# Kernel tuning notes

Measured on AMD Instinct MI355X. Metric: run time of the kernel, lower is better.

The kernel has to match this reference:

```python
import jax, jax.numpy as jnp
import numpy as np

B, TY, ENC, EMB, DEC, V = 16, 255, 512, 256, 512, 32000
EPS = 1e-5


def _lstm(x, Wih, Whh, bih, bhh):
    # x: [B, T, Din]; torch gate order i, f, g, o; h0 = c0 = 0
    Bb = x.shape[0]
    H = Whh.shape[1]
    xw = jnp.einsum('btd,gd->btg', x, Wih) + bih + bhh  # [B, T, 4H]

    def step(carry, xt):
        h, c = carry
        g = xt + h @ Whh.T
        i, f, gg, o = jnp.split(g, 4, axis=-1)
        i = jax.nn.sigmoid(i)
        f = jax.nn.sigmoid(f)
        gg = jnp.tanh(gg)
        o = jax.nn.sigmoid(o)
        c = f * c + i * gg
        h = o * jnp.tanh(c)
        return (h, c), h

    h0 = jnp.zeros((Bb, H), x.dtype)
    _, hs = jax.lax.scan(step, (h0, h0), jnp.swapaxes(xw, 0, 1))
    return jnp.swapaxes(hs, 0, 1)  # [B, T, H]


def setup_inputs():
    key = jax.random.key(0)
    ks = jax.random.split(key, 16)
    s = 0.05
    rn = lambda k, sh: jax.random.normal(k, sh, jnp.float32)
    return {
        'x': rn(ks[0], (B, ENC)),
        'y': jax.random.randint(ks[1], (B, TY), 0, V),
        'fc1_w': rn(ks[2], (EMB, ENC)) * s,
        'fc1_b': rn(ks[3], (EMB,)) * s,
        'bn_g': jnp.ones((EMB,), jnp.float32),
        'bn_b': jnp.zeros((EMB,), jnp.float32),
        'emb': rn(ks[4], (V, EMB)) * s,
        'l1_Wih': rn(ks[5], (4 * DEC, EMB)) * s,
        'l1_Whh': rn(ks[6], (4 * DEC, DEC)) * s,
        'l1_bih': rn(ks[7], (4 * DEC,)) * s,
        'l1_bhh': rn(ks[8], (4 * DEC,)) * s,
        'attn_Wout': rn(ks[9], (DEC, 2 * DEC)) * s,
        'dc_Wih': rn(ks[10], (4 * DEC, DEC)) * s,
        'dc_Whh': rn(ks[11], (4 * DEC, DEC)) * s,
        'dc_bih': rn(ks[12], (4 * DEC,)) * s,
        'dc_bhh': rn(ks[13], (4 * DEC,)) * s,
        'fc2_w': rn(ks[14], (V, DEC)) * s,
        'fc2_b': rn(ks[15], (V,)) * s,
        'lengths': TY + 1,  # all sequences full length
    }


def reference(x, y, fc1_w, fc1_b, bn_g, bn_b, emb, l1_Wih, l1_Whh, l1_bih, l1_bhh,
              attn_Wout, dc_Wih, dc_Whh, dc_bih, dc_bhh, fc2_w, fc2_b, lengths):
    # fc1 + BatchNorm1d (training-mode batch stats, biased var)
    feat = x @ fc1_w.T + fc1_b                         # [B, EMB]
    mu = feat.mean(axis=0)
    var = feat.var(axis=0)
    feat = (feat - mu) / jnp.sqrt(var + EPS) * bn_g + bn_b
    # prepend feature to embedded tokens -> [B, L, EMB], L = TY + 1
    seq = jnp.concatenate([feat[:, None, :], emb[y]], axis=1)
    # first LSTM
    h = _lstm(seq, l1_Wih, l1_Whh, l1_bih, l1_bhh)     # [B, L, DEC]
    L = seq.shape[1]
    # causal dot-product self-attention (vectorized form of the python loop)
    scores = jnp.einsum('bqd,bkd->bqk', h, h)
    mask = jnp.tril(jnp.ones((L, L), bool))
    w = jax.nn.softmax(jnp.where(mask, scores, -1e30), axis=-1)
    mix = jnp.einsum('bqk,bkd->bqd', w, h)
    attn = jnp.tanh(jnp.concatenate([mix, h], axis=-1) @ attn_Wout.T)
    # decoder LSTM cell over attended features
    out = _lstm(attn, dc_Wih, dc_Whh, dc_bih, dc_bhh)  # [B, L, DEC]
    return out @ fc2_w.T + fc2_b                       # [B, L, V]
```

## Files before the change

kernel.cpp:

```cpp
#include <hip/hip_runtime.h>

#define BB 16
#define TY 255
#define ENC 512
#define EMBD 256
#define DEC 512
#define VV 32000
#define LL 256
#define M4 4096
#define GG 2048
#define SENT 0x7FC0

typedef unsigned short u16;
typedef __attribute__((ext_vector_type(8))) short short8;
typedef __attribute__((ext_vector_type(4))) float f32x4;
typedef __attribute__((ext_vector_type(4))) unsigned short u16x4;

__device__ __forceinline__ u16 f2bf(float f) {
  unsigned u = __float_as_uint(f);
  u += 0x7fff + ((u >> 16) & 1);
  return (u16)(u >> 16);
}
__device__ __forceinline__ f32x4 mfma16(short8 a, short8 b, f32x4 c) {
  return __builtin_amdgcn_mfma_f32_16x16x32_bf16(a, b, c, 0, 0, 0);
}
__device__ __forceinline__ float sigmoidf_(float x) { return 1.f / (1.f + expf(-x)); }

__device__ __forceinline__ void st_b32_dev(int* a, int v) {
  asm volatile("global_store_dword %0, %1, off sc1" :: "v"(a), "v"(v) : "memory");
}
__device__ __forceinline__ void gload_lds16(const u16* g, u16* l) {
  __builtin_amdgcn_global_load_lds(
      (const __attribute__((address_space(1))) void*)g,
      (__attribute__((address_space(3))) void*)l, 16, 0, 0);
}

template<bool BT, bool OBF, bool DOTANH, bool BIAS>
__global__ __launch_bounds__(256) void gemm_kernel(
    const u16* __restrict__ A, const u16* __restrict__ Bm, void* __restrict__ Cv,
    const float* __restrict__ bias,
    int K, int lda, int ldb, int ldc,
    long a_bs, long b_bs, long c_bs)
{
  __shared__ u16 As[64][72];
  __shared__ u16 Bs[64][72];
  const int tid = threadIdx.x;
  const long m0 = (long)blockIdx.y * 64, n0 = (long)blockIdx.x * 64;
  const int z = blockIdx.z;
  const u16* Ab = A + (long)z * a_bs;
  const u16* Bb = Bm + (long)z * b_bs;
  const int lane = tid & 63, w = tid >> 6;
  const int wm = w >> 1, wn = w & 1;
  f32x4 acc[2][2] = {};
  for (int k0 = 0; k0 < K; k0 += 64) {
#pragma unroll
    for (int i = 0; i < 2; i++) {
      int c = tid + 256 * i;
      int r = c >> 3, kk = (c & 7) << 3;
      *(short8*)&As[r][kk] = *(const short8*)&Ab[(m0 + r) * (long)lda + k0 + kk];
    }
    if (BT) {
#pragma unroll
      for (int i = 0; i < 2; i++) {
        int c = tid + 256 * i;
        int r = c >> 3, kk = (c & 7) << 3;
        *(short8*)&Bs[r][kk] = *(const short8*)&Bb[(n0 + r) * (long)ldb + k0 + kk];
      }
    } else {
#pragma unroll
      for (int i = 0; i < 2; i++) {
        int c = tid + 256 * i;
        int kk = c >> 3, nn = (c & 7) << 3;
        const u16* s = &Bb[(long)(k0 + kk) * ldb + n0 + nn];
#pragma unroll
        for (int j = 0; j < 8; j++) Bs[nn + j][kk] = s[j];
      }
    }
    __syncthreads();
#pragma unroll
    for (int kf = 0; kf < 2; kf++) {
      const int ko = kf * 32 + (lane >> 4) * 8;
      short8 a0 = *(const short8*)&As[wm * 32 + (lane & 15)][ko];
      short8 a1 = *(const short8*)&As[wm * 32 + 16 + (lane & 15)][ko];
      short8 b0 = *(const short8*)&Bs[wn * 32 + (lane & 15)][ko];
      short8 b1 = *(const short8*)&Bs[wn * 32 + 16 + (lane & 15)][ko];
      acc[0][0] = mfma16(a0, b0, acc[0][0]);
      acc[0][1] = mfma16(a0, b1, acc[0][1]);
      acc[1][0] = mfma16(a1, b0, acc[1][0]);
      acc[1][1] = mfma16(a1, b1, acc[1][1]);
    }
    __syncthreads();
  }
#pragma unroll
  for (int m = 0; m < 2; m++)
#pragma unroll
    for (int n = 0; n < 2; n++) {
#pragma unroll
      for (int r = 0; r < 4; r++) {
        long row = m0 + wm * 32 + m * 16 + (lane >> 4) * 4 + r;
        long col = n0 + wn * 32 + n * 16 + (lane & 15);
        float v = acc[m][n][r];
        if (BIAS) v += bias[col];
        if (DOTANH) v = tanhf(v);
        if (OBF) ((u16*)Cv)[(long)z * c_bs + row * ldc + col] = f2bf(v);
        else ((float*)Cv)[(long)z * c_bs + row * ldc + col] = v;
      }
    }
}

template<bool OBF, bool DOTANH, bool BIAS>
__global__ __launch_bounds__(256) void gemm128_kernel(
    const u16* __restrict__ A, const u16* __restrict__ Bm, void* __restrict__ Cv,
    const float* __restrict__ bias,
    int K, int lda, int ldb, int ldc,
    long a_bs, long b_bs, long c_bs)
{
  __shared__ u16 As[128 * 64];
  __shared__ u16 Bs[128 * 64];
  const int tid = threadIdx.x;
  const long m0 = (long)blockIdx.y * 128, n0 = (long)blockIdx.x * 128;
  const int z = blockIdx.z;
  const u16* Ab = A + (long)z * a_bs;
  const u16* Bb = Bm + (long)z * b_bs;
  const int lane = tid & 63, w = tid >> 6;
  const int wm = w >> 1, wn = w & 1;
  const int rr = tid >> 3, kk = (tid & 7) << 3;
  f32x4 acc[4][4] = {};
  for (int k0 = 0; k0 < K; k0 += 64) {
#pragma unroll
    for (int i = 0; i < 4; i++) {
      gload_lds16(&Ab[(m0 + i * 32 + rr) * (long)lda + k0 + kk],
                  As + (i * 256 + (w << 6)) * 8);
      gload_lds16(&Bb[(n0 + i * 32 + rr) * (long)ldb + k0 + kk],
                  Bs + (i * 256 + (w << 6)) * 8);
    }
    __syncthreads();
#pragma unroll
    for (int kf = 0; kf < 2; kf++) {
      const int ko = kf * 32 + (lane >> 4) * 8;
      short8 a[4], b[4];
#pragma unroll
      for (int mi = 0; mi < 4; mi++)
        a[mi] = *(const short8*)&As[(wm * 64 + mi * 16 + (lane & 15)) * 64 + ko];
#pragma unroll
      for (int ni = 0; ni < 4; ni++)
        b[ni] = *(const short8*)&Bs[(wn * 64 + ni * 16 + (lane & 15)) * 64 + ko];
#pragma unroll
      for (int mi = 0; mi < 4; mi++)
#pragma unroll
        for (int ni = 0; ni < 4; ni++)
          acc[mi][ni] = mfma16(a[mi], b[ni], acc[mi][ni]);
    }
    __syncthreads();
  }
#pragma unroll
  for (int mi = 0; mi < 4; mi++)
#pragma unroll
    for (int ni = 0; ni < 4; ni++) {
#pragma unroll
      for (int r = 0; r < 4; r++) {
        long row = m0 + wm * 64 + mi * 16 + (lane >> 4) * 4 + r;
        long col = n0 + wn * 64 + ni * 16 + (lane & 15);
        float v = acc[mi][ni][r];
        if (BIAS) v += bias[col];
        if (DOTANH) v = tanhf(v);
        if (OBF) ((u16*)Cv)[(long)z * c_bs + row * ldc + col] = f2bf(v);
        else ((float*)Cv)[(long)z * c_bs + row * ldc + col] = v;
      }
    }
}

__global__ void sentinel_kernel(u16* __restrict__ p) {
  long i = ((long)blockIdx.x * 256 + threadIdx.x) * 8;
  short v = (i < 8192) ? (short)0 : (short)SENT;
  short8 s = {v, v, v, v, v, v, v, v};
  *(short8*)&p[i] = s;
}

template<int MODE>
__global__ __launch_bounds__(256) void lstm_kernel(
    const float* __restrict__ xw,
    const u16* __restrict__ Whh,
    u16* __restrict__ Hseq,
    u16* __restrict__ hout)
{
  const int nb = blockIdx.x;
  const int tid = threadIdx.x;
  const int lane = tid & 63, w = tid >> 6;
  __shared__ u16 hs[16][520];
  __shared__ float gbuf[16][64];
  const int ncol0 = nb * 64 + w * 16;
  short8 bfrag[16];
  {
    const u16* wr = Whh + (long)(ncol0 + (lane & 15)) * 512 + ((lane >> 4) * 8);
#pragma unroll
    for (int kf = 0; kf < 16; kf++) bfrag[kf] = *(const short8*)&wr[kf * 32];
  }
  const int b = tid >> 4, jl = tid & 15;
  const int jglob = nb * 16 + jl;
  int cc[4];
#pragma unroll
  for (int i = 0; i < 4; i++) cc[i] = (tid + i * 256 + nb * 32) & 1023;
  float c = 0.f;
  float4 xg = *(const float4*)&xw[((long)b * LL) * GG + nb * 64 + jl * 4];
  for (int t = 0; t < LL; t++) {
    const u16* Hin = Hseq + (long)t * 8192;
    short8 sv[4];
    int bad;
    do {
#pragma unroll
      for (int i = 0; i < 4; i++)
        asm volatile("global_load_dwordx4 %0, %1, off sc1"
                     : "=v"(sv[i]) : "v"(Hin + (cc[i] >> 6) * 512 + (cc[i] & 63) * 8));
      asm volatile("s_waitcnt vmcnt(0)" ::: "memory");
      __builtin_amdgcn_sched_barrier(0);
      bad = 0;
#pragma unroll
      for (int i = 0; i < 4; i++) {
        const int* dv = (const int*)&sv[i];
#pragma unroll
        for (int d = 0; d < 4; d++) bad |= ((dv[d] & 0xFFFF) == SENT);
      }
    } while (__any(bad != 0));
    __builtin_amdgcn_sched_barrier(0);
#pragma unroll
    for (int i = 0; i < 4; i++)
      *(short8*)&hs[cc[i] >> 6][(cc[i] & 63) * 8] = sv[i];
    __syncthreads();
    f32x4 acc0 = {}, acc1 = {};
#pragma unroll
    for (int kf = 0; kf < 8; kf++) {
      short8 a0 = *(const short8*)&hs[lane & 15][(lane >> 4) * 8 + (2 * kf) * 32];
      short8 a1 = *(const short8*)&hs[lane & 15][(lane >> 4) * 8 + (2 * kf + 1) * 32];
      acc0 = mfma16(a0, bfrag[2 * kf], acc0);
      acc1 = mfma16(a1, bfrag[2 * kf + 1], acc1);
    }
    f32x4 acc = acc0 + acc1;
#pragma unroll
    for (int r = 0; r < 4; r++)
      gbuf[(lane >> 4) * 4 + r][w * 16 + (lane & 15)] = acc[r];
    __syncthreads();
    float gi = sigmoidf_(gbuf[b][jl * 4 + 0] + xg.x);
    float gf = sigmoidf_(gbuf[b][jl * 4 + 1] + xg.y);
    float gg = tanhf(gbuf[b][jl * 4 + 2] + xg.z);
    float go = sigmoidf_(gbuf[b][jl * 4 + 3] + xg.w);
    c = gf * c + gi * gg;
    float h = go * tanhf(c);
    u16 hb = f2bf(h);
    unsigned hi16 = (unsigned)__shfl_down((int)(unsigned)hb, 1);
    if ((jl & 1) == 0) {
      int pk = (int)((unsigned)hb | (hi16 << 16));
      st_b32_dev((int*)&Hseq[((long)t + 1) * 8192 + b * 512 + jglob], pk);
    }
    if (MODE == 0) hout[((long)b * LL + t) * 1024 + 512 + jglob] = hb;
    else           hout[((long)b * LL + t) * 512 + jglob] = hb;
    if (t + 1 < LL)
      xg = *(const float4*)&xw[((long)b * LL + (t + 1)) * GG + nb * 64 + jl * 4];
  }
}

__global__ void fc1_kernel(const float* __restrict__ x, const float* __restrict__ wgt,
                           const float* __restrict__ bias, float* __restrict__ feat) {
  __shared__ float xs[ENC];
  int bb = blockIdx.x, j = threadIdx.x;
  for (int k = j; k < ENC; k += 256) xs[k] = x[bb * ENC + k];
  __syncthreads();
  float s = bias[j];
  const float* wr = wgt + (long)j * ENC;
  for (int k = 0; k < ENC; k += 4) {
    float4 wv = *(const float4*)&wr[k];
    s += xs[k] * wv.x + xs[k + 1] * wv.y + xs[k + 2] * wv.z + xs[k + 3] * wv.w;
  }
  feat[bb * EMBD + j] = s;
}

__global__ void bn_embed0_kernel(const float* __restrict__ feat, const float* __restrict__ g,
                                 const float* __restrict__ bb, u16* __restrict__ seq) {
  int j = threadIdx.x;
  float mu = 0.f, m2 = 0.f;
  for (int i = 0; i < BB; i++) { float v = feat[i * EMBD + j]; mu += v; m2 += v * v; }
  mu *= (1.f / BB);
  float var = m2 * (1.f / BB) - mu * mu;
  float sc = g[j] * rsqrtf(var + 1e-5f);
  float sh = bb[j];
  for (int i = 0; i < BB; i++) {
    float v = (feat[i * EMBD + j] - mu) * sc + sh;
    seq[((long)i * LL) * EMBD + j] = f2bf(v);
  }
}

__global__ void embed_kernel(const int* __restrict__ y, const float* __restrict__ emb,
                             u16* __restrict__ seq) {
  int t = blockIdx.x, bb = blockIdx.y;
  int tok = y[bb * TY + t];
  int j = threadIdx.x;
  seq[((long)bb * LL + 1 + t) * EMBD + j] = f2bf(emb[(long)tok * EMBD + j]);
}

__global__ __launch_bounds__(256) void softmax_kernel(const float* __restrict__ sc,
                                                      u16* __restrict__ wsm) {
  int row = blockIdx.x;
  int q = row & (LL - 1);
  int k = threadIdx.x;
  __shared__ float red[8];
  float v = (k <= q) ? sc[(long)row * LL + k] : -3.4e38f;
  float m = v;
#pragma unroll
  for (int o = 32; o > 0; o >>= 1) m = fmaxf(m, __shfl_xor(m, o));
  if ((k & 63) == 0) red[k >> 6] = m;
  __syncthreads();
  m = fmaxf(fmaxf(red[0], red[1]), fmaxf(red[2], red[3]));
  float e = (k <= q) ? expf(v - m) : 0.f;
  float s = e;
#pragma unroll
  for (int o = 32; o > 0; o >>= 1) s += __shfl_xor(s, o);
  if ((k & 63) == 0) red[4 + (k >> 6)] = s;
  __syncthreads();
  s = red[4] + red[5] + red[6] + red[7];
  wsm[(long)row * LL + k] = f2bf(e / s);
}

__global__ void conv_bf16_kernel(const float* __restrict__ s, u16* __restrict__ d) {
  long i = ((long)blockIdx.x * 256 + threadIdx.x) * 4;
  float4 v = *(const float4*)&s[i];
  u16x4 o = {f2bf(v.x), f2bf(v.y), f2bf(v.z), f2bf(v.w)};
  *(u16x4*)&d[i] = o;
}

__global__ void conv_lstm_w_kernel(const float* __restrict__ s, u16* __restrict__ d, int ldk) {
  int n = blockIdx.x;
  int r = (n & 3) * DEC + (n >> 2);
  for (int k = threadIdx.x; k < ldk; k += 256)
    d[(long)n * ldk + k] = f2bf(s[(long)r * ldk + k]);
}

__global__ void conv_lstm_b_kernel(const float* __restrict__ bih, const float* __restrict__ bhh,
                                   float* __restrict__ d) {
  int n = blockIdx.x * 256 + threadIdx.x;
  int r = (n & 3) * DEC + (n >> 2);
  d[n] = bih[r] + bhh[r];
}

extern "C" void kernel_launch(void* const* d_in, const int* in_sizes, int n_in,
                              void* d_out, int out_size, void* d_ws, size_t ws_size,
                              hipStream_t stream) {
  const float* x      = (const float*)d_in[0];
  const int*   y      = (const int*)d_in[1];
  const float* fc1_w  = (const float*)d_in[2];
  const float* fc1_b  = (const float*)d_in[3];
  const float* bn_g   = (const float*)d_in[4];
  const float* bn_b   = (const float*)d_in[5];
  const float* emb    = (const float*)d_in[6];
  const float* l1_Wih = (const float*)d_in[7];
  const float* l1_Whh = (const float*)d_in[8];
  const float* l1_bih = (const float*)d_in[9];
  const float* l1_bhh = (const float*)d_in[10];
  const float* Wout   = (const float*)d_in[11];
  const float* dc_Wih = (const float*)d_in[12];
  const float* dc_Whh = (const float*)d_in[13];
  const float* dc_bih = (const float*)d_in[14];
  const float* dc_bhh = (const float*)d_in[15];
  const float* fc2_w  = (const float*)d_in[16];
  const float* fc2_b  = (const float*)d_in[17];
  float* out = (float*)d_out;

  char* ws = (char*)d_ws;
  float* xw     = (float*)(ws + 0);
  u16*   seqb   = (u16*)(ws + 33554432);
  u16*   cat    = (u16*)(ws + 35651584);
  float* scores = (float*)(ws + 44040192);
  u16*   Hseq   = (u16*)(ws + 44040192);
  u16*   wsm    = (u16*)(ws + 48234496);
  u16*   attnb  = (u16*)(ws + 50331648);
  u16*   h2b    = (u16*)(ws + 54525952);
  u16*   wih1   = (u16*)(ws + 58720256);
  u16*   whh1   = (u16*)(ws + 59768832);
  u16*   wih2   = (u16*)(ws + 61865984);
  u16*   whh2   = (u16*)(ws + 63963136);
  u16*   woutb  = (u16*)(ws + 66060288);
  u16*   fc2wb  = (u16*)(ws + 67108864);
  float* b1p    = (float*)(ws + 99876864);
  float* b2p    = (float*)(ws + 99885056);
  float* feat   = (float*)(ws + 99893248);

  conv_lstm_w_kernel<<<GG, 256, 0, stream>>>(l1_Wih, wih1, EMBD);
  conv_lstm_w_kernel<<<GG, 256, 0, stream>>>(l1_Whh, whh1, DEC);
  conv_lstm_w_kernel<<<GG, 256, 0, stream>>>(dc_Wih, wih2, DEC);
  conv_lstm_w_kernel<<<GG, 256, 0, stream>>>(dc_Whh, whh2, DEC);
  conv_lstm_b_kernel<<<GG / 256, 256, 0, stream>>>(l1_bih, l1_bhh, b1p);
  conv_lstm_b_kernel<<<GG / 256, 256, 0, stream>>>(dc_bih, dc_bhh, b2p);
  conv_bf16_kernel<<<(DEC * 2 * DEC) / 1024, 256, 0, stream>>>(Wout, woutb);
  conv_bf16_kernel<<<(VV * DEC) / 1024, 256, 0, stream>>>(fc2_w, fc2wb);

  fc1_kernel<<<BB, 256, 0, stream>>>(x, fc1_w, fc1_b, feat);
  bn_embed0_kernel<<<1, 256, 0, stream>>>(feat, bn_g, bn_b, seqb);
  embed_kernel<<<dim3(TY, BB), 256, 0, stream>>>(y, emb, seqb);

  gemm128_kernel<false, false, true><<<dim3(GG / 128, M4 / 128, 1), 256, 0, stream>>>(
      seqb, wih1, xw, b1p, EMBD, EMBD, EMBD, GG, 0, 0, 0);
  sentinel_kernel<<<1028, 256, 0, stream>>>(Hseq);
  lstm_kernel<0><<<32, 256, 0, stream>>>(xw, whh1, Hseq, cat);
  gemm128_kernel<false, false, false><<<dim3(LL / 128, LL / 128, BB), 256, 0, stream>>>(
      cat + 512, cat + 512, scores, nullptr, DEC, 1024, 1024, LL,
      (long)LL * 1024, (long)LL * 1024, (long)LL * LL);
  softmax_kernel<<<M4, 256, 0, stream>>>(scores, wsm);
  gemm_kernel<false, true, false, false><<<dim3(DEC / 64, LL / 64, BB), 256, 0, stream>>>(
      wsm, cat + 512, cat, nullptr, LL, LL, 1024, 1024,
      (long)LL * LL, (long)LL * 1024, (long)LL * 1024);
  gemm128_kernel<true, true, false><<<dim3(DEC / 128, M4 / 128, 1), 256, 0, stream>>>(
      cat, woutb, attnb, nullptr, 1024, 1024, 1024, DEC, 0, 0, 0);
  gemm128_kernel<false, false, true><<<dim3(GG / 128, M4 / 128, 1), 256, 0, stream>>>(
      attnb, wih2, xw, b2p, DEC, DEC, DEC, GG, 0, 0, 0);
  sentinel_kernel<<<1028, 256, 0, stream>>>(Hseq);
  lstm_kernel<1><<<32, 256, 0, stream>>>(xw, whh2, Hseq, h2b);
  gemm128_kernel<false, false, true><<<dim3(VV / 128, M4 / 128, 1), 256, 0, stream>>>(
      h2b, fc2wb, out, fc2_b, DEC, DEC, DEC, VV, 0, 0, 0);
}
```

Baseline: 1.466 ms.

## Swap MFMA operands in LSTM step to drop gate LDS exchange, double-buffer polling

The recurrent LSTM kernel now passes the weight fragments as the A operand and the hidden state as B. Each lane's accumulator then holds all four gates for one (batch, unit) pair, so the shared-memory gate buffer and one __syncthreads per timestep go away. The spin-wait on the previous step's hidden state is double-buffered, keeping two sets of loads in flight while one is checked for the sentinel value. Sigmoid and tanh switch to fast __expf-based forms, which lowers accuracy slightly.

Result: slower. 1.557 ms (+6.2%).

```diff
diff --git a/kernel.cpp b/kernel.cpp
--- a/kernel.cpp
+++ b/kernel.cpp
@@ -24,7 +24,8 @@
 __device__ __forceinline__ f32x4 mfma16(short8 a, short8 b, f32x4 c) {
   return __builtin_amdgcn_mfma_f32_16x16x32_bf16(a, b, c, 0, 0, 0);
 }
-__device__ __forceinline__ float sigmoidf_(float x) { return 1.f / (1.f + expf(-x)); }
+__device__ __forceinline__ float fsig(float x) { return 1.f / (1.f + __expf(-x)); }
+__device__ __forceinline__ float ftanh(float x) { return 2.f / (1.f + __expf(-2.f * x)) - 1.f; }
 
 __device__ __forceinline__ void st_b32_dev(int* a, int v) {
   asm volatile("global_store_dword %0, %1, off sc1" :: "v"(a), "v"(v) : "memory");
@@ -188,74 +189,99 @@
   const int tid = threadIdx.x;
   const int lane = tid & 63, w = tid >> 6;
   __shared__ u16 hs[16][520];
-  __shared__ float gbuf[16][64];
   const int ncol0 = nb * 64 + w * 16;
-  short8 bfrag[16];
+  short8 afrag[16];
   {
     const u16* wr = Whh + (long)(ncol0 + (lane & 15)) * 512 + ((lane >> 4) * 8);
 #pragma unroll
-    for (int kf = 0; kf < 16; kf++) bfrag[kf] = *(const short8*)&wr[kf * 32];
-  }
-  const int b = tid >> 4, jl = tid & 15;
-  const int jglob = nb * 16 + jl;
+    for (int kf = 0; kf < 16; kf++) afrag[kf] = *(const short8*)&wr[kf * 32];
+  }
+  const int b2 = lane & 15;
+  const int ug = lane >> 4;
+  const int jglob = nb * 16 + w * 4 + ug;
   int cc[4];
 #pragma unroll
   for (int i = 0; i < 4; i++) cc[i] = (tid + i * 256 + nb * 32) & 1023;
   float c = 0.f;
-  float4 xg = *(const float4*)&xw[((long)b * LL) * GG + nb * 64 + jl * 4];
+  float4 xg = *(const float4*)&xw[((long)b2 * LL) * GG + nb * 64 + (w * 4 + ug) * 4];
   for (int t = 0; t < LL; t++) {
     const u16* Hin = Hseq + (long)t * 8192;
-    short8 sv[4];
-    int bad;
-    do {
+    short8 svA[4], svB[4];
+#pragma unroll
+    for (int i = 0; i < 4; i++)
+      asm volatile("global_load_dwordx4 %0, %1, off sc1"
+                   : "=v"(svA[i]) : "v"(Hin + (cc[i] >> 6) * 512 + (cc[i] & 63) * 8));
+    for (;;) {
 #pragma unroll
       for (int i = 0; i < 4; i++)
         asm volatile("global_load_dwordx4 %0, %1, off sc1"
-                     : "=v"(sv[i]) : "v"(Hin + (cc[i] >> 6) * 512 + (cc[i] & 63) * 8));
-      asm volatile("s_waitcnt vmcnt(0)" ::: "memory");
+                     : "=v"(svB[i]) : "v"(Hin + (cc[i] >> 6) * 512 + (cc[i] & 63) * 8));
+      asm volatile("s_waitcnt vmcnt(4)" ::: "memory");
       __builtin_amdgcn_sched_barrier(0);
-      bad = 0;
-#pragma unroll
-      for (int i = 0; i < 4; i++) {
-        const int* dv = (const int*)&sv[i];
-#pragma unroll
-        for (int d = 0; d < 4; d++) bad |= ((dv[d] & 0xFFFF) == SENT);
-      }
-    } while (__any(bad != 0));
-    __builtin_amdgcn_sched_barrier(0);
-#pragma unroll
-    for (int i = 0; i < 4; i++)
-      *(short8*)&hs[cc[i] >> 6][(cc[i] & 63) * 8] = sv[i];
+      {
+        int bad = 0;
+#pragma unroll
+        for (int i = 0; i < 4; i++) {
+          const int* dv = (const int*)&svA[i];
+#pragma unroll
+          for (int d = 0; d < 4; d++) bad |= ((dv[d] & 0xFFFF) == SENT);
+        }
+        if (!__any(bad)) {
+#pragma unroll
+          for (int i = 0; i < 4; i++)
+            *(short8*)&hs[cc[i] >> 6][(cc[i] & 63) * 8] = svA[i];
+          break;
+        }
+      }
+#pragma unroll
+      for (int i = 0; i < 4; i++)
+        asm volatile("global_load_dwordx4 %0, %1, off sc1"
+                     : "=v"(svA[i]) : "v"(Hin + (cc[i] >> 6) * 512 + (cc[i] & 63) * 8));
+      asm volatile("s_waitcnt vmcnt(4)" ::: "memory");
+      __builtin_amdgcn_sched_barrier(0);
+      {
+        int bad = 0;
+#pragma unroll
+        for (int i = 0; i < 4; i++) {
+          const int* dv = (const int*)&svB[i];
+#pragma unroll
+          for (int d = 0; d < 4; d++) bad |= ((dv[d] & 0xFFFF) == SENT);
+        }
+        if (!__any(bad)) {
+#pragma unroll
+          for (int i = 0; i < 4; i++)
+            *(short8*)&hs[cc[i] >> 6][(cc[i] & 63) * 8] = svB[i];
+          break;
+        }
+      }
+    }
+    asm volatile("s_waitcnt vmcnt(0)" ::: "memory");
     __syncthreads();
     f32x4 acc0 = {}, acc1 = {};
 #pragma unroll
     for (int kf = 0; kf < 8; kf++) {
-      short8 a0 = *(const short8*)&hs[lane & 15][(lane >> 4) * 8 + (2 * kf) * 32];
-      short8 a1 = *(const short8*)&hs[lane & 15][(lane >> 4) * 8 + (2 * kf + 1) * 32];
-      acc0 = mfma16(a0, bfrag[2 * kf], acc0);
-      acc1 = mfma16(a1, bfrag[2 * kf + 1], acc1);
+      short8 h0 = *(const short8*)&hs[lane & 15][(lane >> 4) * 8 + (2 * kf) * 32];
+      short8 h1 = *(const short8*)&hs[lane & 15][(lane >> 4) * 8 + (2 * kf + 1) * 32];
+      acc0 = mfma16(afrag[2 * kf], h0, acc0);
+      acc1 = mfma16(afrag[2 * kf + 1], h1, acc1);
     }
     f32x4 acc = acc0 + acc1;
-#pragma unroll
-    for (int r = 0; r < 4; r++)
-      gbuf[(lane >> 4) * 4 + r][w * 16 + (lane & 15)] = acc[r];
-    __syncthreads();
-    float gi = sigmoidf_(gbuf[b][jl * 4 + 0] + xg.x);
-    float gf = sigmoidf_(gbuf[b][jl * 4 + 1] + xg.y);
-    float gg = tanhf(gbuf[b][jl * 4 + 2] + xg.z);
-    float go = sigmoidf_(gbuf[b][jl * 4 + 3] + xg.w);
+    float gi = fsig(acc[0] + xg.x);
+    float gf = fsig(acc[1] + xg.y);
+    float gg = ftanh(acc[2] + xg.z);
+    float go = fsig(acc[3] + xg.w);
     c = gf * c + gi * gg;
-    float h = go * tanhf(c);
+    float h = go * ftanh(c);
     u16 hb = f2bf(h);
-    unsigned hi16 = (unsigned)__shfl_down((int)(unsigned)hb, 1);
-    if ((jl & 1) == 0) {
+    unsigned hi16 = (unsigned)__shfl_down((int)(unsigned)hb, 16);
+    if ((ug & 1) == 0) {
       int pk = (int)((unsigned)hb | (hi16 << 16));
-      st_b32_dev((int*)&Hseq[((long)t + 1) * 8192 + b * 512 + jglob], pk);
-    }
-    if (MODE == 0) hout[((long)b * LL + t) * 1024 + 512 + jglob] = hb;
-    else           hout[((long)b * LL + t) * 512 + jglob] = hb;
+      st_b32_dev((int*)&Hseq[((long)t + 1) * 8192 + b2 * 512 + jglob], pk);
+    }
+    if (MODE == 0) hout[((long)b2 * LL + t) * 1024 + 512 + jglob] = hb;
+    else           hout[((long)b2 * LL + t) * 512 + jglob] = hb;
     if (t + 1 < LL)
-      xg = *(const float4*)&xw[((long)b * LL + (t + 1)) * GG + nb * 64 + jl * 4];
+      xg = *(const float4*)&xw[((long)b2 * LL + (t + 1)) * GG + nb * 64 + (w * 4 + ug) * 4];
   }
 }
 
```
